# Kernel optimization log

Measured on AMD Instinct MI355X. Metric: run time of the kernel, lower is better.

The kernel has to match this reference:

```python
import jax, jax.numpy as jnp
import numpy as np

MARGIN = 1.0
NUM_CLASSES = 28
K = 16


def setup_inputs() -> dict:
    key = jax.random.key(0)
    k1, k2, k3 = jax.random.split(key, 3)
    B, C, D = 256, 28, 2048
    # multilabel prediction probabilities
    inp = jax.random.uniform(k1, (B, C), dtype=jnp.float32)
    # sparse multilabel targets (p~0.02 so minority-class selection via
    # cumsum(counts) <= 0.5*num_classes is non-degenerate)
    target = jax.random.bernoulli(k2, 0.02, (B, C)).astype(jnp.int32)
    # embeddings used for the mined triplets
    X = jax.random.normal(k3, (B, D), dtype=jnp.float32)
    return {"input": inp, "target": target, "X": X}


def _crl_loss(inp, X, target):
    B = inp.shape[0]
    y = target.astype(inp.dtype)

    # --- get_minority_classes ---
    counts = y.sum(0)                                   # [C] per-class positive counts
    order = jnp.argsort(counts)                         # ascending by count
    cum = jnp.cumsum(counts[order])
    keep_sorted = cum <= 0.5 * NUM_CLASSES              # threshold as in source
    rank = jnp.argsort(order)                           # position of class c in sorted order
    minority = keep_sorted[rank] & (counts > 1)         # [C] bool mask over classes

    # pairwise L1 distances between embeddings: Dm[i,j] = sum_d |X_i - X_j|
    Dm = jnp.abs(X[:, None, :] - X[None, :, :]).sum(-1)  # [B,B]

    pos_mask = target == 1                              # [B,C]
    inf = jnp.inf
    pos_key = jnp.where(pos_mask, inp, inf)             # [B,C] sort keys for positives
    neg_key = jnp.where(pos_mask, -inf, inp)            # [B,C] sort keys for negatives

    def per_class(pk, nk, pm, m_c):
        # hardest negatives of this class: largest predicted prob (neg_idxs[-k:])
        nvals, nidx = jax.lax.top_k(nk, K)              # [K]
        nvalid = jnp.isfinite(nvals).astype(Dm.dtype)
        n_n = nvalid.sum()                              # min(k, n_neg)
        dn_anchor = (Dm[:, nidx] * nvalid).sum(-1)      # [B] sum_j |X_i - X_negj|_1

        def per_anchor(i):
            keys = pk.at[i].set(inf)                    # mask[idx] = 0: exclude anchor
            # hardest positives: smallest predicted prob (sorted[:k])
            pvals, pidx = jax.lax.top_k(-keys, K)
            pvalid = jnp.isfinite(pvals).astype(Dm.dtype)
            n_p = pvalid.sum()                          # min(k, n_pos - 1)
            dp = (Dm[i, pidx] * pvalid).sum()
            w = (pm[i] & m_c).astype(Dm.dtype)          # anchor is a positive of a minority class
            # each positive appears in n_n triplets, each negative in n_p triplets
            return w * n_n * dp, w * n_p * dn_anchor[i]

        dps, dns = jax.vmap(per_anchor)(jnp.arange(B))
        return dps.sum(), dns.sum()

    dp_c, dn_c = jax.vmap(per_class, in_axes=(1, 1, 1, 0))(pos_key, neg_key, pos_mask, minority)
    # TripletLoss with F.l1_loss(size_average=False) sums over all triplet elements,
    # so distance_positive / distance_negative are scalars -> scalar relu loss.
    return jax.nn.relu(dp_c.sum() - dn_c.sum() + MARGIN)


def reference(input, target, X):
    return _crl_loss(input, X, target)
```

## Files before the change

### kernel.cpp

```cpp
#include <hip/hip_runtime.h>
#include <math.h>

typedef unsigned int u32;
typedef unsigned long long u64;

#define BB 256
#define CC 28
#define DD 2048
#define KK 16
#define GA 14
#define NBLK (CC * GA)

struct Meta {
  float acc[2];
  u32 ticket;
  u32 pad;
  int active[CC];
  int mcount[CC];
  int alist[CC][16];
  int slist[CC][16];
  int nlist[CC][16];
};

__global__ __launch_bounds__(256) void k_sel(const float* __restrict__ inp,
                                             const int* __restrict__ target,
                                             Meta* __restrict__ M) {
  const int c = blockIdx.x;
  const int t = threadIdx.x;
  const int wave = t >> 6, lane = t & 63;

  __shared__ u32 s_bits[BB];
  __shared__ u32 s_pb[BB];
  __shared__ int s_cw[4][CC];
  __shared__ int s_counts[CC];
  __shared__ int s_pw[4];

  u32 pb = 0;
  const int4* t4 = (const int4*)(target + t * CC);
#pragma unroll
  for (int k = 0; k < 7; ++k) {
    int4 w = t4[k];
    pb |= (u32)(w.x != 0) << (4 * k) | (u32)(w.y != 0) << (4 * k + 1) |
          (u32)(w.z != 0) << (4 * k + 2) | (u32)(w.w != 0) << (4 * k + 3);
  }
  s_pb[t] = pb;
  const float v = inp[t * CC + c];
  s_bits[t] = __float_as_uint(v);

#pragma unroll
  for (int c2 = 0; c2 < CC; ++c2) {
    u64 b = __ballot((pb >> c2) & 1u);
    if (lane == 0) s_cw[wave][c2] = __popcll(b);
  }
  const int p = (pb >> c) & 1;
  const u64 bp = __ballot(p != 0);
  if (lane == 0) s_pw[wave] = __popcll(bp);
  __syncthreads();
  if (t < CC)
    s_counts[t] = s_cw[0][t] + s_cw[1][t] + s_cw[2][t] + s_cw[3][t];
  __syncthreads();

  const int m = s_counts[c];
  int cum = 0;
#pragma unroll
  for (int c2 = 0; c2 < CC; ++c2) {
    const int m2 = s_counts[c2];
    cum += (m2 < m || (m2 == m && c2 <= c)) ? m2 : 0;
  }
  const bool active = (2 * cum <= CC) && (m > 1);

  if (c == 0 && t == 0) { M->acc[0] = 0.f; M->acc[1] = 0.f; M->ticket = 0u; }
  if (t == 0) { M->active[c] = active ? 1 : 0; M->mcount[c] = m; }
  if (!active) return;

  int rank = 0;
  for (int j = 0; j < BB; ++j) {
    const float vj = __uint_as_float(s_bits[j]);
    const int pj = (s_pb[j] >> c) & 1;
    const bool bpos = (vj < v) || (vj == v && j < t);
    const bool bneg = (vj > v) || (vj == v && j < t);
    rank += p ? ((pj && bpos) ? 1 : 0) : ((!pj && bneg) ? 1 : 0);
  }
  if (p) {
    if (rank < 16) M->slist[c][rank] = t;
    int idx = __popcll(bp & ((1ull << lane) - 1ull));
#pragma unroll
    for (int w2 = 0; w2 < 4; ++w2)
      if (w2 < wave) idx += s_pw[w2];
    if (idx < 16) M->alist[c][idx] = t;
  } else {
    if (rank < KK) M->nlist[c][rank] = t;
  }
}

__global__ __launch_bounds__(256) void k_dist(const float* __restrict__ X,
                                              Meta* __restrict__ M,
                                              float* __restrict__ out) {
  const int c = blockIdx.x;
  const int a = blockIdx.y;
  const int tid = threadIdx.x;
  const int wave = tid >> 6, lane = tid & 63;

  __shared__ int s_S[16], s_N[16];
  __shared__ float s_red[8];

  const int m = M->mcount[c];
  const bool work = (M->active[c] != 0) && (a < m);

  if (work) {
    if (tid < KK) s_N[tid] = M->nlist[c][tid];
    else if (tid >= 64 && tid < 64 + m) s_S[tid - 64] = M->slist[c][tid - 64];
    __syncthreads();

    const int anchor = M->alist[c][a];
    const int NP = m - 1;
    const int NN = min(KK, BB - m);
    int idx_a = 0;
    for (int u = 0; u < m; ++u)
      if (s_S[u] == anchor) idx_a = u;

    const float4* Xa = (const float4*)(X + (size_t)anchor * DD);
    float4 A[8];
#pragma unroll
    for (int q = 0; q < 8; ++q) A[q] = Xa[q * 64 + lane];

    float dp = 0.f, dn = 0.f;
    for (int pidx = wave; pidx < NP + NN; pidx += 4) {
      const bool isdp = pidx < NP;
      const int j = isdp ? s_S[pidx + (pidx >= idx_a ? 1 : 0)] : s_N[pidx - NP];
      const float4* Xj = (const float4*)(X + (size_t)j * DD);
      float partial = 0.f;
#pragma unroll
      for (int q = 0; q < 8; ++q) {
        const float4 b4 = Xj[q * 64 + lane];
        partial += fabsf(A[q].x - b4.x) + fabsf(A[q].y - b4.y) +
                   fabsf(A[q].z - b4.z) + fabsf(A[q].w - b4.w);
      }
#pragma unroll
      for (int s = 1; s < 64; s <<= 1) partial += __shfl_xor(partial, s);
      if (isdp) dp += partial; else dn += partial;
    }
    if (lane == 0) { s_red[2 * wave] = dp; s_red[2 * wave + 1] = dn; }
    __syncthreads();
    if (tid == 0) {
      const float dpT = s_red[0] + s_red[2] + s_red[4] + s_red[6];
      const float dnT = s_red[1] + s_red[3] + s_red[5] + s_red[7];
      atomicAdd(&M->acc[0], (float)NN * dpT);
      atomicAdd(&M->acc[1], (float)NP * dnT);
    }
  }

  if (tid == 0) {
    __threadfence();
    const u32 tk = atomicAdd(&M->ticket, 1u);
    if (tk == (u32)(NBLK - 1)) {
      __threadfence();
      const float a0 = atomicAdd(&M->acc[0], 0.f);
      const float a1 = atomicAdd(&M->acc[1], 0.f);
      out[0] = fmaxf(a0 - a1 + 1.0f, 0.0f);
    }
  }
}

extern "C" void kernel_launch(void* const* d_in, const int* in_sizes, int n_in,
                              void* d_out, int out_size, void* d_ws, size_t ws_size,
                              hipStream_t stream) {
  (void)in_sizes; (void)n_in; (void)out_size; (void)ws_size;
  const float* inp    = (const float*)d_in[0];
  const int*   target = (const int*)d_in[1];
  const float* X      = (const float*)d_in[2];
  float* out = (float*)d_out;
  Meta* M = (Meta*)d_ws;

  k_sel<<<CC, 256, 0, stream>>>(inp, target, M);
  k_dist<<<dim3(CC, GA), 256, 0, stream>>>(X, M, out);
}
```

Before: 85.32 us.

## Fuse selection and distance kernels into one launch with per-block recomputed selection

```diff
diff --git a/kernel.cpp b/kernel.cpp
--- a/kernel.cpp
+++ b/kernel.cpp
@@ -9,154 +9,145 @@
 #define DD 2048
 #define KK 16
 #define GA 14
-#define NBLK (CC * GA)
 
-struct Meta {
+struct Sync {
   float acc[2];
   u32 ticket;
   u32 pad;
-  int active[CC];
-  int mcount[CC];
-  int alist[CC][16];
-  int slist[CC][16];
-  int nlist[CC][16];
 };
 
-__global__ __launch_bounds__(256) void k_sel(const float* __restrict__ inp,
-                                             const int* __restrict__ target,
-                                             Meta* __restrict__ M) {
+__global__ __launch_bounds__(256) void k_main(const float* __restrict__ inp,
+                                              const int* __restrict__ target,
+                                              const float* __restrict__ X,
+                                              Sync* __restrict__ S,
+                                              float* __restrict__ out) {
   const int c = blockIdx.x;
-  const int t = threadIdx.x;
-  const int wave = t >> 6, lane = t & 63;
+  const int a = blockIdx.y;
+  const int tid = threadIdx.x;
+  const int wave = tid >> 6, lane = tid & 63;
 
   __shared__ u32 s_bits[BB];
   __shared__ u32 s_pb[BB];
   __shared__ int s_cw[4][CC];
   __shared__ int s_counts[CC];
+  __shared__ int s_act[CC];
   __shared__ int s_pw[4];
+  __shared__ int s_S[16], s_N[16], s_anchor;
+  __shared__ float s_red[8];
 
   u32 pb = 0;
-  const int4* t4 = (const int4*)(target + t * CC);
+  const int4* t4 = (const int4*)(target + tid * CC);
 #pragma unroll
   for (int k = 0; k < 7; ++k) {
     int4 w = t4[k];
     pb |= (u32)(w.x != 0) << (4 * k) | (u32)(w.y != 0) << (4 * k + 1) |
           (u32)(w.z != 0) << (4 * k + 2) | (u32)(w.w != 0) << (4 * k + 3);
   }
-  s_pb[t] = pb;
-  const float v = inp[t * CC + c];
-  s_bits[t] = __float_as_uint(v);
+  s_pb[tid] = pb;
+  const u32 b = __float_as_uint(inp[tid * CC + c]);
+  s_bits[tid] = b;
 
 #pragma unroll
   for (int c2 = 0; c2 < CC; ++c2) {
-    u64 b = __ballot((pb >> c2) & 1u);
-    if (lane == 0) s_cw[wave][c2] = __popcll(b);
+    u64 bl = __ballot((pb >> c2) & 1u);
+    if (lane == 0) s_cw[wave][c2] = __popcll(bl);
   }
   const int p = (pb >> c) & 1;
   const u64 bp = __ballot(p != 0);
   if (lane == 0) s_pw[wave] = __popcll(bp);
   __syncthreads();
-  if (t < CC)
-    s_counts[t] = s_cw[0][t] + s_cw[1][t] + s_cw[2][t] + s_cw[3][t];
+  if (tid < CC)
+    s_counts[tid] = s_cw[0][tid] + s_cw[1][tid] + s_cw[2][tid] + s_cw[3][tid];
+  __syncthreads();
+
+  if (tid < CC) {
+    const int mt = s_counts[tid];
+    int cum = 0;
+#pragma unroll
+    for (int c2 = 0; c2 < CC; ++c2) {
+      const int m2 = s_counts[c2];
+      cum += (m2 < mt || (m2 == mt && c2 <= tid)) ? m2 : 0;
+    }
+    s_act[tid] = ((2 * cum <= CC) && (mt > 1)) ? mt : 0;
+  }
   __syncthreads();
 
   const int m = s_counts[c];
-  int cum = 0;
+  const bool active = (s_act[c] > 0) && (a < m);
+  int total = 0;
+  if (tid == 0) {
 #pragma unroll
-  for (int c2 = 0; c2 < CC; ++c2) {
-    const int m2 = s_counts[c2];
-    cum += (m2 < m || (m2 == m && c2 <= c)) ? m2 : 0;
+    for (int c2 = 0; c2 < CC; ++c2) total += s_act[c2];
   }
-  const bool active = (2 * cum <= CC) && (m > 1);
 
-  if (c == 0 && t == 0) { M->acc[0] = 0.f; M->acc[1] = 0.f; M->ticket = 0u; }
-  if (t == 0) { M->active[c] = active ? 1 : 0; M->mcount[c] = m; }
-  if (!active) return;
+  if (!active) {
+    if (c == 0 && a == 0 && tid == 0 && total == 0)
+      out[0] = 1.0f;
+    return;
+  }
 
   int rank = 0;
   for (int j = 0; j < BB; ++j) {
-    const float vj = __uint_as_float(s_bits[j]);
+    const u32 bj = s_bits[j];
     const int pj = (s_pb[j] >> c) & 1;
-    const bool bpos = (vj < v) || (vj == v && j < t);
-    const bool bneg = (vj > v) || (vj == v && j < t);
+    const bool bpos = (bj < b) || (bj == b && j < tid);
+    const bool bneg = (bj > b) || (bj == b && j < tid);
     rank += p ? ((pj && bpos) ? 1 : 0) : ((!pj && bneg) ? 1 : 0);
   }
   if (p) {
-    if (rank < 16) M->slist[c][rank] = t;
+    if (rank < 16) s_S[rank] = tid;
     int idx = __popcll(bp & ((1ull << lane) - 1ull));
 #pragma unroll
     for (int w2 = 0; w2 < 4; ++w2)
       if (w2 < wave) idx += s_pw[w2];
-    if (idx < 16) M->alist[c][idx] = t;
+    if (idx == a) s_anchor = tid;
   } else {
-    if (rank < KK) M->nlist[c][rank] = t;
+    if (rank < KK) s_N[rank] = tid;
   }
-}
+  __syncthreads();
 
-__global__ __launch_bounds__(256) void k_dist(const float* __restrict__ X,
-                                              Meta* __restrict__ M,
-                                              float* __restrict__ out) {
-  const int c = blockIdx.x;
-  const int a = blockIdx.y;
-  const int tid = threadIdx.x;
-  const int wave = tid >> 6, lane = tid & 63;
+  const int anchor = s_anchor;
+  const int NP = m - 1;
+  const int NN = min(KK, BB - m);
+  int idx_a = 0;
+  for (int u = 0; u < m; ++u)
+    if (s_S[u] == anchor) idx_a = u;
 
-  __shared__ int s_S[16], s_N[16];
-  __shared__ float s_red[8];
+  const float4* Xa = (const float4*)(X + (size_t)anchor * DD);
+  float4 A[8];
+#pragma unroll
+  for (int q = 0; q < 8; ++q) A[q] = Xa[q * 64 + lane];
 
-  const int m = M->mcount[c];
-  const bool work = (M->active[c] != 0) && (a < m);
-
-  if (work) {
-    if (tid < KK) s_N[tid] = M->nlist[c][tid];
-    else if (tid >= 64 && tid < 64 + m) s_S[tid - 64] = M->slist[c][tid - 64];
-    __syncthreads();
-
-    const int anchor = M->alist[c][a];
-    const int NP = m - 1;
-    const int NN = min(KK, BB - m);
-    int idx_a = 0;
-    for (int u = 0; u < m; ++u)
-      if (s_S[u] == anchor) idx_a = u;
-
-    const float4* Xa = (const float4*)(X + (size_t)anchor * DD);
-    float4 A[8];
+  float dp = 0.f, dn = 0.f;
+  for (int pidx = wave; pidx < NP + NN; pidx += 4) {
+    const bool isdp = pidx < NP;
+    const int j = isdp ? s_S[pidx + (pidx >= idx_a ? 1 : 0)] : s_N[pidx - NP];
+    const float4* Xj = (const float4*)(X + (size_t)j * DD);
+    float partial = 0.f;
 #pragma unroll
-    for (int q = 0; q < 8; ++q) A[q] = Xa[q * 64 + lane];
-
-    float dp = 0.f, dn = 0.f;
-    for (int pidx = wave; pidx < NP + NN; pidx += 4) {
-      const bool isdp = pidx < NP;
-      const int j = isdp ? s_S[pidx + (pidx >= idx_a ? 1 : 0)] : s_N[pidx - NP];
-      const float4* Xj = (const float4*)(X + (size_t)j * DD);
-      float partial = 0.f;
+    for (int q = 0; q < 8; ++q) {
+      const float4 b4 = Xj[q * 64 + lane];
+      partial += fabsf(A[q].x - b4.x) + fabsf(A[q].y - b4.y) +
+                 fabsf(A[q].z - b4.z) + fabsf(A[q].w - b4.w);
+    }
 #pragma unroll
-      for (int q = 0; q < 8; ++q) {
-        const float4 b4 = Xj[q * 64 + lane];
-        partial += fabsf(A[q].x - b4.x) + fabsf(A[q].y - b4.y) +
-                   fabsf(A[q].z - b4.z) + fabsf(A[q].w - b4.w);
-      }
-#pragma unroll
-      for (int s = 1; s < 64; s <<= 1) partial += __shfl_xor(partial, s);
-      if (isdp) dp += partial; else dn += partial;
-    }
-    if (lane == 0) { s_red[2 * wave] = dp; s_red[2 * wave + 1] = dn; }
-    __syncthreads();
-    if (tid == 0) {
-      const float dpT = s_red[0] + s_red[2] + s_red[4] + s_red[6];
-      const float dnT = s_red[1] + s_red[3] + s_red[5] + s_red[7];
-      atomicAdd(&M->acc[0], (float)NN * dpT);
-      atomicAdd(&M->acc[1], (float)NP * dnT);
-    }
+    for (int s = 1; s < 64; s <<= 1) partial += __shfl_xor(partial, s);
+    if (isdp) dp += partial; else dn += partial;
   }
+  if (lane == 0) { s_red[2 * wave] = dp; s_red[2 * wave + 1] = dn; }
+  __syncthreads();
 
   if (tid == 0) {
+    const float dpT = s_red[0] + s_red[2] + s_red[4] + s_red[6];
+    const float dnT = s_red[1] + s_red[3] + s_red[5] + s_red[7];
+    atomicAdd(&S->acc[0], (float)NN * dpT);
+    atomicAdd(&S->acc[1], (float)NP * dnT);
     __threadfence();
-    const u32 tk = atomicAdd(&M->ticket, 1u);
-    if (tk == (u32)(NBLK - 1)) {
+    const u32 tk = atomicAdd(&S->ticket, 1u);
+    if (tk == (u32)(total - 1)) {
       __threadfence();
-      const float a0 = atomicAdd(&M->acc[0], 0.f);
-      const float a1 = atomicAdd(&M->acc[1], 0.f);
+      const float a0 = atomicAdd(&S->acc[0], 0.f);
+      const float a1 = atomicAdd(&S->acc[1], 0.f);
       out[0] = fmaxf(a0 - a1 + 1.0f, 0.0f);
     }
   }
@@ -170,8 +161,8 @@
   const int*   target = (const int*)d_in[1];
   const float* X      = (const float*)d_in[2];
   float* out = (float*)d_out;
-  Meta* M = (Meta*)d_ws;
+  Sync* S = (Sync*)d_ws;
 
-  k_sel<<<CC, 256, 0, stream>>>(inp, target, M);
-  k_dist<<<dim3(CC, GA), 256, 0, stream>>>(X, M, out);
+  hipMemsetAsync(S, 0, sizeof(Sync), stream);
+  k_main<<<dim3(CC, GA), 256, 0, stream>>>(inp, target, X, S, out);
 }
```

Result: faster. 82.75 us (-3.0%).
